# Performance work log

Hardware: AMD Instinct MI355X
Metric: run time of the kernel (lower is better)

Reference implementation:

```python
import jax, jax.numpy as jnp
import numpy as np
from jax import lax

B, N, S = 16, 8192, 512
BASE_K = 16
MS_K = (8, 16, 24)


def _fps(xyz, npoint):
    # farthest point sampling; xyz [B,N,3] -> indices [B,npoint]
    b, n, _ = xyz.shape
    def body(carry, _):
        dists, far = carry
        c = jnp.take_along_axis(xyz, far[:, None, None], axis=1)  # [B,1,3]
        d = jnp.sum((xyz - c) ** 2, -1)
        dists = jnp.minimum(dists, d)
        return (dists, jnp.argmax(dists, -1).astype(jnp.int32)), far
    init = (jnp.full((b, n), 1e10, xyz.dtype), jnp.zeros((b,), jnp.int32))
    _, idx = lax.scan(body, init, None, length=npoint)
    return idx.swapaxes(0, 1)  # [B,npoint]


def _sqdist(a, b):
    # a [B,S,3], b [B,N,3] -> squared distances [B,S,N] (same topk order as cdist)
    return (jnp.sum(a * a, -1)[:, :, None] + jnp.sum(b * b, -1)[:, None, :]
            - 2.0 * jnp.einsum('bsc,bnc->bsn', a, b))


def _gather(pts, idx):
    # pts [B,N,C], idx [B,S,K] -> [B,S,K,C]
    b = pts.shape[0]
    return pts[jnp.arange(b)[:, None, None], idx]


def setup_inputs():
    key = jax.random.key(0)
    ks = jax.random.split(key, 6)
    s = 0.05
    return {
        'l0_xyz': jax.random.normal(ks[0], (B, 3, N), jnp.float32),
        'l0_points': jax.random.normal(ks[1], (B, 3, N), jnp.float32),
        'sa_W1': jax.random.normal(ks[2], (64, 6), jnp.float32) * s,
        'sa_b1': jnp.zeros((64,), jnp.float32),
        'sa_W2': jax.random.normal(ks[3], (128, 64), jnp.float32) * s,
        'sa_b2': jnp.zeros((128,), jnp.float32),
        'ms_W1': jax.random.normal(ks[4], (3, 64, 3), jnp.float32) * s,
        'ms_b1': jnp.zeros((3, 64), jnp.float32),
        'ms_W2': jax.random.normal(ks[5], (3, 128, 64), jnp.float32) * s,
        'ms_b2': jnp.zeros((3, 128), jnp.float32),
    }


def reference(l0_xyz, l0_points, sa_W1, sa_b1, sa_W2, sa_b2, ms_W1, ms_b1, ms_W2, ms_b2):
    xyz = l0_xyz.swapaxes(1, 2)     # [B,N,3]
    pts = l0_points.swapaxes(1, 2)  # [B,N,3]
    # --- PointNet_SA_Module_KNN: FPS + KNN grouping + shared MLP + max-pool ---
    fps_idx = _fps(lax.stop_gradient(xyz), S)                         # [B,S]
    new_xyz = jnp.take_along_axis(xyz, fps_idx[:, :, None], axis=1)  # [B,S,3]
    d = _sqdist(lax.stop_gradient(new_xyz), lax.stop_gradient(xyz))  # [B,S,N]
    _, knn_idx = lax.top_k(-d, BASE_K)                                # [B,S,K]
    g_xyz = _gather(xyz, knn_idx) - new_xyz[:, :, None]               # [B,S,K,3]
    g_pts = _gather(pts, knn_idx)                                     # [B,S,K,3]
    feat = jnp.concatenate([g_xyz, g_pts], -1)                        # [B,S,K,6]
    h = jax.nn.relu(jnp.einsum('bskc,oc->bsko', feat, sa_W1) + sa_b1)
    h = jnp.einsum('bsko,po->bskp', h, sa_W2) + sa_b2
    base_feat = jnp.max(h, axis=2)                                    # [B,S,128]
    keypoints = new_xyz.swapaxes(1, 2)                                # [B,3,S]
    # --- multi-scale: no_grad cdist, per-scale topk + rel-coord MLP + max-pool ---
    dist = _sqdist(lax.stop_gradient(new_xyz), lax.stop_gradient(xyz))  # [B,S,N]
    feats = [base_feat.swapaxes(1, 2)]                                  # [B,128,S]
    for i, k in enumerate(MS_K):
        k_eff = min(k, N)
        _, idx = lax.top_k(-dist, k_eff)                                # [B,S,k]
        rel = _gather(xyz, idx) - new_xyz[:, :, None]                   # [B,S,k,3]
        h = jax.nn.relu(jnp.einsum('bskc,oc->bsko', rel, ms_W1[i]) + ms_b1[i])
        h = jnp.einsum('bsko,po->bskp', h, ms_W2[i]) + ms_b2[i]
        feats.append(jnp.max(h, axis=2).swapaxes(1, 2))                 # [B,128,S]
    return keypoints, jnp.concatenate(feats, axis=1)                    # [B,3,S],[B,512,S]
```

## Files before the change

kernel.cpp:

```cpp
#include <hip/hip_runtime.h>

#define BB 16
#define NN 8192
#define SS 512
#define N3 (3 * NN)
#define KD 14

typedef unsigned short u16;
typedef unsigned int u32;
typedef unsigned long long u64;
typedef float v2f __attribute__((ext_vector_type(2)));

__device__ __forceinline__ v2f pk_add(v2f a, v2f b) {
  v2f r;
  asm("v_pk_add_f32 %0, %1, %2" : "=v"(r) : "v"(a), "v"(b));
  return r;
}
__device__ __forceinline__ v2f pk_mul(v2f a, v2f b) {
  v2f r;
  asm("v_pk_mul_f32 %0, %1, %2" : "=v"(r) : "v"(a), "v"(b));
  return r;
}

template <int CTRL>
__device__ __forceinline__ u64 dpp_maxk(u64 k) {
  u32 lo = (u32)k, hi = (u32)(k >> 32);
  u32 slo = (u32)__builtin_amdgcn_update_dpp(0, (int)lo, CTRL, 0xf, 0xf, false);
  u32 shi = (u32)__builtin_amdgcn_update_dpp(0, (int)hi, CTRL, 0xf, 0xf, false);
  u64 s = ((u64)shi << 32) | (u64)slo;
  return (s > k) ? s : k;
}
template <int CTRL>
__device__ __forceinline__ u64 dpp_mink(u64 k) {
  u32 lo = (u32)k, hi = (u32)(k >> 32);
  u32 slo = (u32)__builtin_amdgcn_update_dpp((int)lo, (int)lo, CTRL, 0xf, 0xf, false);
  u32 shi = (u32)__builtin_amdgcn_update_dpp((int)hi, (int)hi, CTRL, 0xf, 0xf, false);
  u64 s = ((u64)shi << 32) | (u64)slo;
  return (s < k) ? s : k;
}
__device__ __forceinline__ u64 maxk(u64 a, u64 b) { return (a > b) ? a : b; }

__global__ __launch_bounds__(256) void k_prep(const float* __restrict__ xyz,
                                              const float* __restrict__ pts,
                                              float4* __restrict__ xyz4,
                                              float4* __restrict__ pts4) {
  int i = blockIdx.x * 256 + threadIdx.x;
  int b = i >> 13, n = i & (NN - 1);
  const float* xb = xyz + b * N3;
  float x = xb[n], y = xb[NN + n], z = xb[2 * NN + n];
  float w = __fadd_rn(__fadd_rn(__fmul_rn(x, x), __fmul_rn(y, y)), __fmul_rn(z, z));
  xyz4[i] = make_float4(x, y, z, w);
  const float* pb = pts + b * N3;
  pts4[i] = make_float4(pb[n], pb[NN + n], pb[2 * NN + n], 0.f);
}

__global__ __attribute__((amdgpu_flat_work_group_size(512, 512),
                          amdgpu_waves_per_eu(2, 2)))
void k_fps(const float* __restrict__ xyz, float* __restrict__ out_kp) {
  __shared__ float sxyz[NN * 3];
  __shared__ int sIdx[SS];
  __shared__ u64 rkey[2][8];
  int b = blockIdx.x, t = threadIdx.x;
  const float* base = xyz + b * N3;
  v2f px[8], py[8], pz[8], dm[8];
#pragma unroll
  for (int j = 0; j < 8; ++j) {
    int n0 = j * 1024 + t, n1 = n0 + 512;
    px[j] = v2f{base[n0], base[n1]};
    py[j] = v2f{base[NN + n0], base[NN + n1]};
    pz[j] = v2f{base[2 * NN + n0], base[2 * NN + n1]};
    dm[j] = v2f{1e10f, 1e10f};
    sxyz[n0 * 3 + 0] = px[j].x;
    sxyz[n0 * 3 + 1] = py[j].x;
    sxyz[n0 * 3 + 2] = pz[j].x;
    sxyz[n1 * 3 + 0] = px[j].y;
    sxyz[n1 * 3 + 1] = py[j].y;
    sxyz[n1 * 3 + 2] = pz[j].y;
  }
#pragma unroll
  for (int j = 0; j < 8; ++j) {
    asm volatile("" : "+v"(px[j]), "+v"(py[j]), "+v"(pz[j]));
  }
  float cx = base[0], cy = base[NN], cz = base[2 * NN];
  int far = 0;
  int lane = t & 63, w = t >> 6;
  u32 tb = (u32)(NN - t);
  for (int it = 0; it < SS; ++it) {
    if (t == 0) sIdx[it] = far;
    v2f ncx = v2f{-cx, -cx}, ncy = v2f{-cy, -cy}, ncz = v2f{-cz, -cz};
    float vmax = 0.0f;
#pragma unroll
    for (int j = 0; j < 8; ++j) {
      v2f dx = pk_add(px[j], ncx);
      v2f dy = pk_add(py[j], ncy);
      v2f dz = pk_add(pz[j], ncz);
      v2f xx = pk_mul(dx, dx);
      v2f yy = pk_mul(dy, dy);
      v2f s = pk_add(xx, yy);
      v2f zz = pk_mul(dz, dz);
      v2f d = pk_add(s, zz);
      float a0 = fminf(dm[j].x, d.x);
      float a1 = fminf(dm[j].y, d.y);
      dm[j].x = a0;
      dm[j].y = a1;
      vmax = fmaxf(vmax, fmaxf(a0, a1));
    }
    u32 cand = 0;
#pragma unroll
    for (int j = 7; j >= 0; --j) {
      u32 v1 = tb - (u32)(j * 1024 + 512);
      u32 v0 = tb - (u32)(j * 1024);
      cand = (dm[j].y == vmax) ? v1 : cand;
      cand = (dm[j].x == vmax) ? v0 : cand;
    }
    u64 key = ((u64)__float_as_uint(vmax) << 32) | cand;
    key = dpp_maxk<0x111>(key);
    key = dpp_maxk<0x112>(key);
    key = dpp_maxk<0x114>(key);
    key = dpp_maxk<0x118>(key);
    key = dpp_maxk<0x142>(key);
    key = dpp_maxk<0x143>(key);
    int pb = it & 1;
    if (lane == 63) rkey[pb][w] = key;
    __syncthreads();
    u64 k0 = rkey[pb][0], k1 = rkey[pb][1];
    u64 k2 = rkey[pb][2], k3 = rkey[pb][3];
    u64 k4 = rkey[pb][4], k5 = rkey[pb][5];
    u64 k6 = rkey[pb][6], k7 = rkey[pb][7];
    u64 kg = maxk(maxk(maxk(k0, k1), maxk(k2, k3)),
                  maxk(maxk(k4, k5), maxk(k6, k7)));
    far = NN - (int)(u32)(kg & 0xffffffffu);
    cx = sxyz[far * 3 + 0];
    cy = sxyz[far * 3 + 1];
    cz = sxyz[far * 3 + 2];
  }
  __syncthreads();
  for (int i = t; i < SS; i += 512) {
    int id = sIdx[i];
    out_kp[b * 1536 + i] = base[id];
    out_kp[b * 1536 + SS + i] = base[NN + id];
    out_kp[b * 1536 + 2 * SS + i] = base[2 * NN + id];
  }
}

template <int USE4>
__global__ __launch_bounds__(256) void k_knn(const float* __restrict__ xyz,
                                             const float4* __restrict__ xyz4,
                                             const float* __restrict__ kp,
                                             u16* __restrict__ knn) {
  int t = threadIdx.x;
  int row = blockIdx.x * 4 + (t >> 6);
  int lane = t & 63;
  int b = row >> 9, s = row & (SS - 1);
  const float* base = xyz + b * N3;
  const float4* base4 = xyz4 + (b << 13);
  float ax = kp[b * 1536 + s];
  float ay = kp[b * 1536 + SS + s];
  float az = kp[b * 1536 + 2 * SS + s];
  float aw = __fadd_rn(__fadd_rn(__fmul_rn(ax, ax), __fmul_rn(ay, ay)), __fmul_rn(az, az));
  u64 arr[KD];
#pragma unroll
  for (int i = 0; i < KD; ++i) arr[i] = ~0ull;
  for (int c = 0; c < 128; ++c) {
    int n = c * 64 + lane;
    float qx, qy, qz, qw;
    if constexpr (USE4) {
      float4 q = base4[n];
      qx = q.x; qy = q.y; qz = q.z; qw = q.w;
    } else {
      qx = base[n]; qy = base[NN + n]; qz = base[2 * NN + n];
      qw = __fadd_rn(__fadd_rn(__fmul_rn(qx, qx), __fmul_rn(qy, qy)), __fmul_rn(qz, qz));
    }
    float dot = __fadd_rn(__fadd_rn(__fmul_rn(ax, qx), __fmul_rn(ay, qy)), __fmul_rn(az, qz));
    float d = __fsub_rn(__fadd_rn(aw, qw), __fmul_rn(2.0f, dot));
    u32 ub = __float_as_uint(d);
    ub ^= (ub & 0x80000000u) ? 0xFFFFFFFFu : 0x80000000u;
    u64 key = ((u64)ub << 32) | (u32)n;
    if (key < arr[KD - 1]) {
      bool cg[KD];
#pragma unroll
      for (int i = 0; i < KD; ++i) cg[i] = arr[i] > key;
#pragma unroll
      for (int i = KD - 1; i >= 1; --i)
        arr[i] = cg[i - 1] ? arr[i - 1] : (cg[i] ? key : arr[i]);
      arr[0] = cg[0] ? key : arr[0];
    }
  }
  u64 mine = 0;
  for (int it = 0; it < 24; ++it) {
    u64 m = arr[0];
    m = dpp_mink<0x111>(m);
    m = dpp_mink<0x112>(m);
    m = dpp_mink<0x114>(m);
    m = dpp_mink<0x118>(m);
    m = dpp_mink<0x142>(m);
    m = dpp_mink<0x143>(m);
    u32 mlo = (u32)__builtin_amdgcn_readlane((int)(u32)m, 63);
    u32 mhi = (u32)__builtin_amdgcn_readlane((int)(u32)(m >> 32), 63);
    u64 mw = ((u64)mhi << 32) | (u64)mlo;
    if (lane == it) mine = mw;
    if (arr[0] == mw) {
#pragma unroll
      for (int i = 0; i < KD - 1; ++i) arr[i] = arr[i + 1];
      arr[KD - 1] = ~0ull;
    }
  }
  if (lane < 24) knn[row * 24 + lane] = (u16)(mine & 0xFFFFu);
}

template <int USE4>
__global__ __launch_bounds__(256) void k_mlp(
    const float* __restrict__ xyz, const float* __restrict__ pts,
    const float4* __restrict__ xyz4, const float4* __restrict__ pts4,
    const float* __restrict__ kp, const u16* __restrict__ knn,
    const float* __restrict__ W1, const float* __restrict__ b1,
    const float* __restrict__ W2, const float* __restrict__ b2,
    const float* __restrict__ msW1, const float* __restrict__ msb1,
    const float* __restrict__ msW2, const float* __restrict__ msb2,
    float* __restrict__ out) {
  __shared__ float smem[6688];
  int t = threadIdx.x, lane = t & 63, w = t >> 6;
  int b = blockIdx.x >> 6, s0 = (blockIdx.x & 63) * 8;
  if (blockIdx.y == 0) {
    float* sW1T = smem;
    float* sb1 = smem + 384;
    float* sfeat = smem + 448;
    float* sh1 = smem + 832;
    for (int i = t; i < 384; i += 256) {
      int o = i / 6, c = i - o * 6;
      sW1T[c * 64 + o] = W1[i];
    }
    if (t < 64) sb1[t] = b1[t];
    float wgtA[64], wgtB[64];
#pragma unroll
    for (int j = 0; j < 64; ++j) {
      wgtA[j] = W2[lane * 64 + j];
      wgtB[j] = W2[(lane + 64) * 64 + j];
    }
    float b2A = b2[lane], b2B = b2[lane + 64];
    __syncthreads();
    for (int g = 0; g < 2; ++g) {
      if (t < 128) {
        int p = t >> 1, h = t & 1;
        int rr = p >> 4, k = p & 15;
        int s = s0 + g * 4 + rr, row = b * SS + s;
        int id = knn[row * 24 + k];
        float* f = &sfeat[rr * 96 + k * 6];
        if (h == 0) {
          float qx, qy, qz;
          if constexpr (USE4) {
            float4 q = xyz4[(b << 13) + id];
            qx = q.x; qy = q.y; qz = q.z;
          } else {
            qx = xyz[b * N3 + id];
            qy = xyz[b * N3 + NN + id];
            qz = xyz[b * N3 + 2 * NN + id];
          }
          f[0] = __fsub_rn(qx, kp[b * 1536 + s]);
          f[1] = __fsub_rn(qy, kp[b * 1536 + SS + s]);
          f[2] = __fsub_rn(qz, kp[b * 1536 + 2 * SS + s]);
        } else {
          float px_, py_, pz_;
          if constexpr (USE4) {
            float4 q = pts4[(b << 13) + id];
            px_ = q.x; py_ = q.y; pz_ = q.z;
          } else {
            px_ = pts[b * N3 + id];
            py_ = pts[b * N3 + NN + id];
            pz_ = pts[b * N3 + 2 * NN + id];
          }
          f[3] = px_;
          f[4] = py_;
          f[5] = pz_;
        }
      }
      __syncthreads();
#pragma unroll
      for (int m = 0; m < 16; ++m) {
        int u = m * 256 + t;
        int rr = u >> 10, rem = u & 1023, k = rem >> 6, o = rem & 63;
        float acc = sb1[o];
#pragma unroll
        for (int c = 0; c < 6; ++c) acc = fmaf(sfeat[rr * 96 + k * 6 + c], sW1T[c * 64 + o], acc);
        sh1[rr * 1024 + k * 64 + o] = fmaxf(acc, 0.f);
      }
      __syncthreads();
      float bestA = -1e30f, bestB = -1e30f;
#pragma unroll
      for (int k = 0; k < 16; ++k) {
        const float4* h4 = (const float4*)&sh1[w * 1024 + k * 64];
        float a0 = 0.f, a1 = 0.f;
#pragma unroll
        for (int j = 0; j < 16; ++j) {
          float4 hv = h4[j];
          a0 = fmaf(hv.x, wgtA[4 * j], a0);
          a0 = fmaf(hv.y, wgtA[4 * j + 1], a0);
          a0 = fmaf(hv.z, wgtA[4 * j + 2], a0);
          a0 = fmaf(hv.w, wgtA[4 * j + 3], a0);
          a1 = fmaf(hv.x, wgtB[4 * j], a1);
          a1 = fmaf(hv.y, wgtB[4 * j + 1], a1);
          a1 = fmaf(hv.z, wgtB[4 * j + 2], a1);
          a1 = fmaf(hv.w, wgtB[4 * j + 3], a1);
        }
        bestA = fmaxf(bestA, a0);
        bestB = fmaxf(bestB, a1);
      }
      int s = s0 + g * 4 + w;
      out[24576 + b * 262144 + lane * 512 + s] = bestA + b2A;
      out[24576 + b * 262144 + (lane + 64) * 512 + s] = bestB + b2B;
      __syncthreads();
    }
  } else {
    int scale = blockIdx.y - 1;
    int kk = 8 * (scale + 1);
    float* sW1T = smem;
    float* sb1 = smem + 192;
    float* sfeat = smem + 256;
    float* sh1 = smem + 544;
    const float* W1s = msW1 + scale * 192;
    for (int i = t; i < 192; i += 256) {
      int o = i / 3, c = i - o * 3;
      sW1T[c * 64 + o] = W1s[i];
    }
    if (t < 64) sb1[t] = msb1[scale * 64 + t];
    float wgtA[64], wgtB[64];
#pragma unroll
    for (int j = 0; j < 64; ++j) {
      wgtA[j] = msW2[scale * 8192 + lane * 64 + j];
      wgtB[j] = msW2[scale * 8192 + (lane + 64) * 64 + j];
    }
    float b2A = msb2[scale * 128 + lane], b2B = msb2[scale * 128 + lane + 64];
    __syncthreads();
    int co = 128 * (scale + 1);
    for (int g = 0; g < 2; ++g) {
      if (t < 96) {
        int rr = t / 24, k = t - rr * 24;
        int s = s0 + g * 4 + rr, row = b * SS + s;
        int id = knn[row * 24 + k];
        float qx, qy, qz;
        if constexpr (USE4) {
          float4 q = xyz4[(b << 13) + id];
          qx = q.x; qy = q.y; qz = q.z;
        } else {
          qx = xyz[b * N3 + id];
          qy = xyz[b * N3 + NN + id];
          qz = xyz[b * N3 + 2 * NN + id];
        }
        float* f = &sfeat[rr * 72 + k * 3];
        f[0] = __fsub_rn(qx, kp[b * 1536 + s]);
        f[1] = __fsub_rn(qy, kp[b * 1536 + SS + s]);
        f[2] = __fsub_rn(qz, kp[b * 1536 + 2 * SS + s]);
      }
      __syncthreads();
      for (int rr = 0; rr < 4; ++rr) {
        for (int u = t; u < kk * 64; u += 256) {
          int k = u >> 6, o = u & 63;
          float acc = sb1[o];
          acc = fmaf(sfeat[rr * 72 + k * 3 + 0], sW1T[o], acc);
          acc = fmaf(sfeat[rr * 72 + k * 3 + 1], sW1T[64 + o], acc);
          acc = fmaf(sfeat[rr * 72 + k * 3 + 2], sW1T[128 + o], acc);
          sh1[rr * 1536 + k * 64 + o] = fmaxf(acc, 0.f);
        }
      }
      __syncthreads();
      float bestA = -1e30f, bestB = -1e30f;
      for (int k = 0; k < kk; ++k) {
        const float4* h4 = (const float4*)&sh1[w * 1536 + k * 64];
        float a0 = 0.f, a1 = 0.f;
#pragma unroll
        for (int j = 0; j < 16; ++j) {
          float4 hv = h4[j];
          a0 = fmaf(hv.x, wgtA[4 * j], a0);
          a0 = fmaf(hv.y, wgtA[4 * j + 1], a0);
          a0 = fmaf(hv.z, wgtA[4 * j + 2], a0);
          a0 = fmaf(hv.w, wgtA[4 * j + 3], a0);
          a1 = fmaf(hv.x, wgtB[4 * j], a1);
          a1 = fmaf(hv.y, wgtB[4 * j + 1], a1);
          a1 = fmaf(hv.z, wgtB[4 * j + 2], a1);
          a1 = fmaf(hv.w, wgtB[4 * j + 3], a1);
        }
        bestA = fmaxf(bestA, a0);
        bestB = fmaxf(bestB, a1);
      }
      int s = s0 + g * 4 + w;
      out[24576 + b * 262144 + (co + lane) * 512 + s] = bestA + b2A;
      out[24576 + b * 262144 + (co + lane + 64) * 512 + s] = bestB + b2B;
      __syncthreads();
    }
  }
}

extern "C" void kernel_launch(void* const* d_in, const int* in_sizes, int n_in,
                              void* d_out, int out_size, void* d_ws, size_t ws_size,
                              hipStream_t stream) {
  const float* xyz = (const float*)d_in[0];
  const float* pts = (const float*)d_in[1];
  const float* sa_W1 = (const float*)d_in[2];
  const float* sa_b1 = (const float*)d_in[3];
  const float* sa_W2 = (const float*)d_in[4];
  const float* sa_b2 = (const float*)d_in[5];
  const float* ms_W1 = (const float*)d_in[6];
  const float* ms_b1 = (const float*)d_in[7];
  const float* ms_W2 = (const float*)d_in[8];
  const float* ms_b2 = (const float*)d_in[9];
  float* out = (float*)d_out;
  const float* kp = (const float*)d_out;

  u16* knn = (u16*)d_ws;
  float4* xyz4 = (float4*)((char*)d_ws + 393216);
  float4* pts4 = xyz4 + BB * NN;
  const size_t need4 = 393216 + (size_t)2 * BB * NN * sizeof(float4);
  const bool use4 = ws_size >= need4;

  if (use4) k_prep<<<BB * NN / 256, 256, 0, stream>>>(xyz, pts, xyz4, pts4);
  k_fps<<<BB, 512, 0, stream>>>(xyz, out);
  if (use4) {
    k_knn<1><<<(BB * SS) / 4, 256, 0, stream>>>(xyz, xyz4, kp, knn);
    k_mlp<1><<<dim3(BB * 64, 4), 256, 0, stream>>>(xyz, pts, xyz4, pts4, kp, knn,
                                                   sa_W1, sa_b1, sa_W2, sa_b2,
                                                   ms_W1, ms_b1, ms_W2, ms_b2, out);
  } else {
    k_knn<0><<<(BB * SS) / 4, 256, 0, stream>>>(xyz, xyz4, kp, knn);
    k_mlp<0><<<dim3(BB * 64, 4), 256, 0, stream>>>(xyz, pts, xyz4, pts4, kp, knn,
                                                   sa_W1, sa_b1, sa_W2, sa_b2,
                                                   ms_W1, ms_b1, ms_W2, ms_b2, out);
  }
}
```

Baseline: 985.5 us.

## Split each KNN query across a 4-wave block with shallower per-lane lists

The KNN kernel now assigns one 256-thread block per query row instead of one wave. Each lane scans 32 points and keeps a 7-deep sorted candidate list instead of scanning 128 points with a 14-deep list. Each wave extracts its top 24 with DPP min-reductions, and wave 0 merges the 96 results through shared memory. This shortens the serial scan and insertion work per lane and raises parallelism, at the cost of an extra merge stage, a block barrier and a shallower per-lane buffer that could drop true neighbours if more than 7 of them land in one lane.

Measured after the change: 904.3 us. 1.09x faster.

```diff
diff --git a/kernel.cpp b/kernel.cpp
--- a/kernel.cpp
+++ b/kernel.cpp
@@ -5,6 +5,7 @@
 #define SS 512
 #define N3 (3 * NN)
 #define KD 14
+#define KDB 7
 
 typedef unsigned short u16;
 typedef unsigned int u32;
@@ -39,6 +40,18 @@
   return (s < k) ? s : k;
 }
 __device__ __forceinline__ u64 maxk(u64 a, u64 b) { return (a > b) ? a : b; }
+
+__device__ __forceinline__ u64 wave_min_u64(u64 m) {
+  m = dpp_mink<0x111>(m);
+  m = dpp_mink<0x112>(m);
+  m = dpp_mink<0x114>(m);
+  m = dpp_mink<0x118>(m);
+  m = dpp_mink<0x142>(m);
+  m = dpp_mink<0x143>(m);
+  u32 mlo = (u32)__builtin_amdgcn_readlane((int)(u32)m, 63);
+  u32 mhi = (u32)__builtin_amdgcn_readlane((int)(u32)(m >> 32), 63);
+  return ((u64)mhi << 32) | (u64)mlo;
+}
 
 __global__ __launch_bounds__(256) void k_prep(const float* __restrict__ xyz,
                                               const float* __restrict__ pts,
@@ -143,17 +156,77 @@
   }
 }
 
-template <int USE4>
-__global__ __launch_bounds__(256) void k_knn(const float* __restrict__ xyz,
-                                             const float4* __restrict__ xyz4,
-                                             const float* __restrict__ kp,
-                                             u16* __restrict__ knn) {
+__global__ __launch_bounds__(256) void k_knn_blk(const float4* __restrict__ xyz4,
+                                                 const float* __restrict__ kp,
+                                                 u16* __restrict__ knn) {
+  __shared__ u64 skeys[96];
+  int t = threadIdx.x, lane = t & 63, w = t >> 6;
+  int b = blockIdx.x >> 9, s = blockIdx.x & (SS - 1);
+  const float4* base4 = xyz4 + (b << 13);
+  float ax = kp[b * 1536 + s];
+  float ay = kp[b * 1536 + SS + s];
+  float az = kp[b * 1536 + 2 * SS + s];
+  float aw = __fadd_rn(__fadd_rn(__fmul_rn(ax, ax), __fmul_rn(ay, ay)), __fmul_rn(az, az));
+  u64 arr[KDB];
+#pragma unroll
+  for (int i = 0; i < KDB; ++i) arr[i] = ~0ull;
+  for (int c = 0; c < 32; ++c) {
+    int n = c * 256 + t;
+    float4 q = base4[n];
+    float dot = __fadd_rn(__fadd_rn(__fmul_rn(ax, q.x), __fmul_rn(ay, q.y)),
+                          __fmul_rn(az, q.z));
+    float d = __fsub_rn(__fadd_rn(aw, q.w), __fmul_rn(2.0f, dot));
+    u32 ub = __float_as_uint(d);
+    ub ^= (ub & 0x80000000u) ? 0xFFFFFFFFu : 0x80000000u;
+    u64 key = ((u64)ub << 32) | (u32)n;
+    if (key < arr[KDB - 1]) {
+      bool cg[KDB];
+#pragma unroll
+      for (int i = 0; i < KDB; ++i) cg[i] = arr[i] > key;
+#pragma unroll
+      for (int i = KDB - 1; i >= 1; --i)
+        arr[i] = cg[i - 1] ? arr[i - 1] : (cg[i] ? key : arr[i]);
+      arr[0] = cg[0] ? key : arr[0];
+    }
+  }
+  u64 mine = 0;
+  for (int it = 0; it < 24; ++it) {
+    u64 mw = wave_min_u64(arr[0]);
+    if (lane == it) mine = mw;
+    if (arr[0] == mw) {
+#pragma unroll
+      for (int i = 0; i < KDB - 1; ++i) arr[i] = arr[i + 1];
+      arr[KDB - 1] = ~0ull;
+    }
+  }
+  if (lane < 24) skeys[w * 24 + lane] = mine;
+  __syncthreads();
+  if (w == 0) {
+    u64 a = skeys[lane];
+    u64 b2 = (lane < 32) ? skeys[64 + lane] : ~0ull;
+    u64 lo = (a < b2) ? a : b2;
+    u64 hi = (a < b2) ? b2 : a;
+    u64 outk = 0;
+    for (int it = 0; it < 24; ++it) {
+      u64 mw = wave_min_u64(lo);
+      if (lane == it) outk = mw;
+      if (lo == mw) {
+        lo = hi;
+        hi = ~0ull;
+      }
+    }
+    if (lane < 24) knn[blockIdx.x * 24 + lane] = (u16)(outk & 0xFFFFu);
+  }
+}
+
+__global__ __launch_bounds__(256) void k_knn_solo(const float* __restrict__ xyz,
+                                                  const float* __restrict__ kp,
+                                                  u16* __restrict__ knn) {
   int t = threadIdx.x;
   int row = blockIdx.x * 4 + (t >> 6);
   int lane = t & 63;
   int b = row >> 9, s = row & (SS - 1);
   const float* base = xyz + b * N3;
-  const float4* base4 = xyz4 + (b << 13);
   float ax = kp[b * 1536 + s];
   float ay = kp[b * 1536 + SS + s];
   float az = kp[b * 1536 + 2 * SS + s];
@@ -163,14 +236,8 @@
   for (int i = 0; i < KD; ++i) arr[i] = ~0ull;
   for (int c = 0; c < 128; ++c) {
     int n = c * 64 + lane;
-    float qx, qy, qz, qw;
-    if constexpr (USE4) {
-      float4 q = base4[n];
-      qx = q.x; qy = q.y; qz = q.z; qw = q.w;
-    } else {
-      qx = base[n]; qy = base[NN + n]; qz = base[2 * NN + n];
-      qw = __fadd_rn(__fadd_rn(__fmul_rn(qx, qx), __fmul_rn(qy, qy)), __fmul_rn(qz, qz));
-    }
+    float qx = base[n], qy = base[NN + n], qz = base[2 * NN + n];
+    float qw = __fadd_rn(__fadd_rn(__fmul_rn(qx, qx), __fmul_rn(qy, qy)), __fmul_rn(qz, qz));
     float dot = __fadd_rn(__fadd_rn(__fmul_rn(ax, qx), __fmul_rn(ay, qy)), __fmul_rn(az, qz));
     float d = __fsub_rn(__fadd_rn(aw, qw), __fmul_rn(2.0f, dot));
     u32 ub = __float_as_uint(d);
@@ -188,16 +255,7 @@
   }
   u64 mine = 0;
   for (int it = 0; it < 24; ++it) {
-    u64 m = arr[0];
-    m = dpp_mink<0x111>(m);
-    m = dpp_mink<0x112>(m);
-    m = dpp_mink<0x114>(m);
-    m = dpp_mink<0x118>(m);
-    m = dpp_mink<0x142>(m);
-    m = dpp_mink<0x143>(m);
-    u32 mlo = (u32)__builtin_amdgcn_readlane((int)(u32)m, 63);
-    u32 mhi = (u32)__builtin_amdgcn_readlane((int)(u32)(m >> 32), 63);
-    u64 mw = ((u64)mhi << 32) | (u64)mlo;
+    u64 mw = wave_min_u64(arr[0]);
     if (lane == it) mine = mw;
     if (arr[0] == mw) {
 #pragma unroll
@@ -415,12 +473,12 @@
   if (use4) k_prep<<<BB * NN / 256, 256, 0, stream>>>(xyz, pts, xyz4, pts4);
   k_fps<<<BB, 512, 0, stream>>>(xyz, out);
   if (use4) {
-    k_knn<1><<<(BB * SS) / 4, 256, 0, stream>>>(xyz, xyz4, kp, knn);
+    k_knn_blk<<<BB * SS, 256, 0, stream>>>(xyz4, kp, knn);
     k_mlp<1><<<dim3(BB * 64, 4), 256, 0, stream>>>(xyz, pts, xyz4, pts4, kp, knn,
                                                    sa_W1, sa_b1, sa_W2, sa_b2,
                                                    ms_W1, ms_b1, ms_W2, ms_b2, out);
   } else {
-    k_knn<0><<<(BB * SS) / 4, 256, 0, stream>>>(xyz, xyz4, kp, knn);
+    k_knn_solo<<<(BB * SS) / 4, 256, 0, stream>>>(xyz, kp, knn);
     k_mlp<0><<<dim3(BB * 64, 4), 256, 0, stream>>>(xyz, pts, xyz4, pts4, kp, knn,
                                                    sa_W1, sa_b1, sa_W2, sa_b2,
                                                    ms_W1, ms_b1, ms_W2, ms_b2, out);
```
